# Kernel tuning notes

Hardware: AMD Instinct MI355X
Metric: run time of the kernel (lower is better)

The kernel has to match this reference:

```python
import jax, jax.numpy as jnp
import numpy as np

B, T, C = 2, 2048, 1024
H = 16
HS = C // H  # 64
LN_EPS = 1e-5

def setup_inputs() -> dict:
    key = jax.random.key(0)
    ks = jax.random.split(key, 12)
    s = lambda *sh: 0.02
    inp = {
        'x': jax.random.normal(ks[0], (B, T, C), jnp.float32),
        # per-head Q/K/V weights (bias=False), stacked over heads: [H, C, HS]
        'wq': jax.random.normal(ks[1], (H, C, HS), jnp.float32) * 0.02,
        'wk': jax.random.normal(ks[2], (H, C, HS), jnp.float32) * 0.02,
        'wv': jax.random.normal(ks[3], (H, C, HS), jnp.float32) * 0.02,
        'w_proj': jax.random.normal(ks[4], (C, C), jnp.float32) * 0.02,
        'b_proj': jnp.zeros((C,), jnp.float32),
        'w1': jax.random.normal(ks[5], (C, 4 * C), jnp.float32) * 0.02,
        'b1': jnp.zeros((4 * C,), jnp.float32),
        'w2': jax.random.normal(ks[6], (4 * C, C), jnp.float32) * 0.02,
        'b2': jnp.zeros((C,), jnp.float32),
        'ln1_g': jnp.ones((C,), jnp.float32),
        'ln1_b': jnp.zeros((C,), jnp.float32),
        'ln2_g': jnp.ones((C,), jnp.float32),
        'ln2_b': jnp.zeros((C,), jnp.float32),
    }
    return inp

def _layernorm(x, g, b):
    mu = jnp.mean(x, axis=-1, keepdims=True)
    var = jnp.mean(jnp.square(x - mu), axis=-1, keepdims=True)
    return (x - mu) * jax.lax.rsqrt(var + LN_EPS) * g + b

def reference(x, wq, wk, wv, w_proj, b_proj, w1, b1, w2, b2, ln1_g, ln1_b, ln2_g, ln2_b):
    Bx, Tx, Cx = x.shape
    h = _layernorm(x, ln1_g, ln1_b)
    q = jnp.einsum('btc,hcd->bhtd', h, wq)
    k = jnp.einsum('btc,hcd->bhtd', h, wk)
    v = jnp.einsum('btc,hcd->bhtd', h, wv)
    # NOTE: original scales by n_embedding**-0.5 (C), not head_size**-0.5
    scores = jnp.einsum('bhtd,bhsd->bhts', q, k) * (Cx ** -0.5)
    causal = jnp.tril(jnp.ones((Tx, Tx), bool))
    scores = jnp.where(causal, scores, -jnp.inf)
    att = jax.nn.softmax(scores, axis=-1)  # [B,H,T,T]
    out = jnp.einsum('bhts,bhsd->bhtd', att, v)
    out = out.transpose(0, 2, 1, 3).reshape(Bx, Tx, Cx)  # concat heads
    out = out @ w_proj + b_proj
    x = x + out
    h2 = _layernorm(x, ln2_g, ln2_b)
    ff = jax.nn.relu(h2 @ w1 + b1) @ w2 + b2
    return x + ff
```

## Files before the change

### kernel.cpp

```cpp
#include <hip/hip_runtime.h>
#include <hip/hip_bf16.h>
#include <stdint.h>

typedef __bf16 bf16_t;
typedef __bf16 bf16x8 __attribute__((ext_vector_type(8)));
typedef __bf16 bf16x4 __attribute__((ext_vector_type(4)));
typedef float f32x4 __attribute__((ext_vector_type(4)));

static constexpr int TT = 2048, CC = 1024;

__device__ __forceinline__ void gld_lds16(const void* g, void* l) {
  __builtin_amdgcn_global_load_lds((const __attribute__((address_space(1))) void*)g,
                                   (__attribute__((address_space(3))) void*)l, 16, 0, 0);
}

__global__ __launch_bounds__(256) void prep_all(const float* __restrict__ wq,
                                                const float* __restrict__ wk,
                                                const float* __restrict__ wv,
                                                const float* __restrict__ wproj,
                                                const float* __restrict__ w1,
                                                const float* __restrict__ w2,
                                                bf16_t* __restrict__ Bqkv,
                                                bf16_t* __restrict__ Bproj,
                                                bf16_t* __restrict__ B1w,
                                                bf16_t* __restrict__ B2w,
                                                const float* __restrict__ x,
                                                const float* __restrict__ g,
                                                const float* __restrict__ b,
                                                bf16_t* __restrict__ h1out) {
  const int id = blockIdx.x;
  const int tid = threadIdx.x;
  if (id >= 12288) {
    const int row = id - 12288;
    const float4 v = ((const float4*)(x + (size_t)row * CC))[tid];
    float s = v.x + v.y + v.z + v.w;
    float q = v.x * v.x + v.y * v.y + v.z * v.z + v.w * v.w;
#pragma unroll
    for (int off = 1; off < 64; off <<= 1) {
      s += __shfl_xor(s, off);
      q += __shfl_xor(q, off);
    }
    __shared__ float red[8];
    const int wave = tid >> 6, lane = tid & 63;
    if (lane == 0) { red[wave] = s; red[4 + wave] = q; }
    __syncthreads();
    s = red[0] + red[1] + red[2] + red[3];
    q = red[4] + red[5] + red[6] + red[7];
    const float mu = s * (1.0f / CC);
    float var = q * (1.0f / CC) - mu * mu;
    var = fmaxf(var, 0.f);
    const float rstd = rsqrtf(var + 1e-5f);
    const float4 gv = ((const float4*)g)[tid];
    const float4 bv = ((const float4*)b)[tid];
    bf16x4 o;
    o[0] = (bf16_t)((v.x - mu) * rstd * gv.x + bv.x);
    o[1] = (bf16_t)((v.y - mu) * rstd * gv.y + bv.y);
    o[2] = (bf16_t)((v.z - mu) * rstd * gv.z + bv.z);
    o[3] = (bf16_t)((v.w - mu) * rstd * gv.w + bv.w);
    *(bf16x4*)(h1out + (size_t)row * CC + tid * 4) = o;
    return;
  }
  const float* in;
  bf16_t* out;
  int K, N, kb, nb;
  if (id < 3072) {
    const int which = id >> 10;
    const int r = id & 1023;
    const int z = r >> 6;
    const int rr = r & 63;
    kb = rr >> 1;
    nb = rr & 1;
    K = 1024; N = 64;
    const float* srcs[3] = {wq, wk, wv};
    in = srcs[which] + (size_t)z * 1024 * 64;
    out = Bqkv + (size_t)which * 1024 * 1024 + (size_t)z * 1024 * 64;
  } else if (id < 4096) {
    const int r = id - 3072;
    kb = r >> 5; nb = r & 31;
    K = 1024; N = 1024;
    in = wproj; out = Bproj;
  } else if (id < 8192) {
    const int r = id - 4096;
    kb = r & 31; nb = r >> 5;
    K = 1024; N = 4096;
    in = w1; out = B1w;
  } else {
    const int r = id - 8192;
    kb = r >> 5; nb = r & 31;
    K = 4096; N = 1024;
    in = w2; out = B2w;
  }
  __shared__ float t[32][33];
  const int tx = tid & 31, ty = tid >> 5;
  const int k0 = kb * 32, n0 = nb * 32;
#pragma unroll
  for (int j = 0; j < 4; ++j)
    t[ty + j * 8][tx] = in[(size_t)(k0 + ty + j * 8) * N + n0 + tx];
  __syncthreads();
#pragma unroll
  for (int j = 0; j < 4; ++j)
    out[(size_t)(n0 + ty + j * 8) * K + k0 + tx] = (bf16_t)t[tx][ty + j * 8];
}

__global__ __launch_bounds__(256) void ln_f32_bf16(const float* __restrict__ x,
                                                   const float* __restrict__ g,
                                                   const float* __restrict__ b,
                                                   bf16_t* __restrict__ out) {
  const int row = blockIdx.x;
  const int tid = threadIdx.x;
  const float4 v = ((const float4*)(x + (size_t)row * CC))[tid];
  float s = v.x + v.y + v.z + v.w;
  float q = v.x * v.x + v.y * v.y + v.z * v.z + v.w * v.w;
#pragma unroll
  for (int off = 1; off < 64; off <<= 1) {
    s += __shfl_xor(s, off);
    q += __shfl_xor(q, off);
  }
  __shared__ float red[8];
  const int wave = tid >> 6, lane = tid & 63;
  if (lane == 0) { red[wave] = s; red[4 + wave] = q; }
  __syncthreads();
  s = red[0] + red[1] + red[2] + red[3];
  q = red[4] + red[5] + red[6] + red[7];
  const float mu = s * (1.0f / CC);
  float var = q * (1.0f / CC) - mu * mu;
  var = fmaxf(var, 0.f);
  const float rstd = rsqrtf(var + 1e-5f);
  const float4 gv = ((const float4*)g)[tid];
  const float4 bv = ((const float4*)b)[tid];
  bf16x4 o;
  o[0] = (bf16_t)((v.x - mu) * rstd * gv.x + bv.x);
  o[1] = (bf16_t)((v.y - mu) * rstd * gv.y + bv.y);
  o[2] = (bf16_t)((v.z - mu) * rstd * gv.z + bv.z);
  o[3] = (bf16_t)((v.w - mu) * rstd * gv.w + bv.w);
  *(bf16x4*)(out + (size_t)row * CC + tid * 4) = o;
}

template <int EPI, int BM, int BN, int DEPTH, int NW>
__global__ __launch_bounds__(NW * 64) void gemm_bt(const bf16_t* __restrict__ A,
                                                   const bf16_t* __restrict__ Bt,
                                                   void* __restrict__ Cout,
                                                   const float* __restrict__ bias,
                                                   const float* __restrict__ res,
                                                   bf16_t* __restrict__ vt,
                                                   int M, int N, int K) {
  constexpr int WSN = (NW == 8) ? 4 : 2;
  constexpr int WM = BM / 2, WN = BN / WSN;
  constexpr int MF = WM / 16, NF = WN / 16;
  constexpr int WROWS = NW * 8;
  constexpr int NA = BM / WROWS, NB = BN / WROWS;
  __shared__ alignas(16) bf16_t As[DEPTH][BM * 64];
  __shared__ alignas(16) bf16_t Bs[DEPTH][BN * 64];
  const int tid = threadIdx.x;
  const int wave = tid >> 6, lane = tid & 63;
  const int lr = lane & 15, lg = lane >> 4;
  const int wm = wave / WSN, wn = wave % WSN;

  const int gx = gridDim.x;
  const int nwg = gx * gridDim.y;
  const int orig = (int)blockIdx.y * gx + (int)blockIdx.x;
  const int wgid = (orig & 7) * (nwg >> 3) + (orig >> 3);
  const int tm0 = (wgid / gx) * BM, tn0 = (wgid % gx) * BN;

  const int sr = lane >> 3;
  const int scs = (lane & 7) ^ sr;
  const bf16_t* Ag[NA];
#pragma unroll
  for (int i = 0; i < NA; ++i)
    Ag[i] = A + (size_t)(tm0 + i * WROWS + wave * 8 + sr) * K + scs * 8;
  const bf16_t* Bg[NB];
#pragma unroll
  for (int i = 0; i < NB; ++i)
    Bg[i] = Bt + (size_t)(tn0 + i * WROWS + wave * 8 + sr) * K + scs * 8;

  auto STAGE = [&](int k0, int buf) {
#pragma unroll
    for (int i = 0; i < NA; ++i)
      gld_lds16(Ag[i] + k0, &As[buf][(i * WROWS + wave * 8) * 64]);
#pragma unroll
    for (int i = 0; i < NB; ++i)
      gld_lds16(Bg[i] + k0, &Bs[buf][(i * WROWS + wave * 8) * 64]);
  };

  f32x4 acc[MF][NF] = {};
  const int NT = K >> 6;

  STAGE(0, 0);
  asm volatile("s_waitcnt vmcnt(0)" ::: "memory");
  __builtin_amdgcn_s_barrier();

  for (int t = 0; t < NT; ++t) {
    const int cur = t % DEPTH;
    const bf16_t* Ac = As[cur];
    const bf16_t* Bc = Bs[cur];
    const bool more = (t + DEPTH - 1) < NT;
    if (more) STAGE((t + DEPTH - 1) << 6, (t + DEPTH - 1) % DEPTH);

    __builtin_amdgcn_s_setprio(1);
#pragma unroll
    for (int kk = 0; kk < 2; ++kk) {
      const int ch = ((kk * 4 + lg) ^ (lr & 7)) * 8;
      bf16x8 af[MF], bfr[NF];
#pragma unroll
      for (int n = 0; n < NF; ++n)
        bfr[n] = *(const bf16x8*)&Bc[(wn * WN + n * 16 + lr) * 64 + ch];
#pragma unroll
      for (int m = 0; m < MF; ++m)
        af[m] = *(const bf16x8*)&Ac[(wm * WM + m * 16 + lr) * 64 + ch];
#pragma unroll
      for (int m = 0; m < MF; ++m)
#pragma unroll
        for (int n = 0; n < NF; ++n)
          acc[m][n] =
              __builtin_amdgcn_mfma_f32_16x16x32_bf16(af[m], bfr[n], acc[m][n], 0, 0, 0);
    }
    __builtin_amdgcn_s_setprio(0);
    asm volatile("s_waitcnt vmcnt(0)" ::: "memory");
    __builtin_amdgcn_sched_barrier(0);
    __builtin_amdgcn_s_barrier();
  }

#pragma unroll
  for (int m = 0; m < MF; ++m) {
#pragma unroll
    for (int i = 0; i < 4; ++i) {
      const int row = tm0 + wm * WM + m * 16 + lg * 4 + i;
#pragma unroll
      for (int n = 0; n < NF; ++n) {
        const int col = tn0 + wn * WN + n * 16 + lr;
        float v = acc[m][n][i];
        if (EPI == 1) v = fmaxf(v + bias[col], 0.f);
        if (EPI == 2) v = v + bias[col] + res[(size_t)row * N + col];
        if (EPI == 2) {
          ((float*)Cout)[(size_t)row * N + col] = v;
        } else if (EPI == 3) {
          if (col >= 2048) {
            const int hd = col - 2048;
            const size_t vidx =
                ((size_t)((row >> 11) * 16 + (hd >> 6)) * 64 + (hd & 63)) * TT + (row & (TT - 1));
            vt[vidx] = (bf16_t)v;
          } else {
            ((bf16_t*)Cout)[(size_t)row * N + col] = (bf16_t)v;
          }
        } else {
          ((bf16_t*)Cout)[(size_t)row * N + col] = (bf16_t)v;
        }
      }
    }
  }
}

__global__ __launch_bounds__(256, 3) void attn_fwd(const bf16_t* __restrict__ qkv,
                                                   const bf16_t* __restrict__ Vt,
                                                   bf16_t* __restrict__ O) {
  const int bh = blockIdx.x;
  const int bb = bh >> 4, hh = bh & 15;
  const int qt = 31 - (int)blockIdx.y;
  const int qbase = qt * 64;
  const int tid = threadIdx.x;
  const int wave = tid >> 6, lane = tid & 63;
  const int lr = lane & 15, lg = lane >> 4;
  const bf16_t* Qp = qkv + (size_t)bb * TT * 3072 + hh * 64;
  const bf16_t* Kp = Qp + 1024;
  const bf16_t* Vh = Vt + (size_t)bh * 64 * TT;

  constexpr int KLP = 72;
  constexpr int VLP = 136;
  constexpr int PLP = 136;
  __shared__ alignas(16) bf16_t Klds[128 * KLP];
  __shared__ alignas(16) bf16_t Vlds[64 * VLP];
  __shared__ alignas(16) bf16_t PlS[4][16 * PLP];
  bf16_t* Pw = PlS[wave];

  const int ksr = wave * 32 + (lane >> 3);
  const int ksc = (lane & 7) * 8;
  const int vsr = wave * 16 + (lane >> 4);
  const int vsc = (lane & 15) * 8;

  const int qrow = qbase + wave * 16;
  bf16x8 qf0, qf1;
  {
    const bf16x8 a = *(const bf16x8*)(Qp + (size_t)(qrow + lr) * 3072 + lg * 8);
    const bf16x8 b = *(const bf16x8*)(Qp + (size_t)(qrow + lr) * 3072 + 32 + lg * 8);
#pragma unroll
    for (int j = 0; j < 8; ++j) {
      qf0[j] = (bf16_t)((float)a[j] * 0.03125f);
      qf1[j] = (bf16_t)((float)b[j] * 0.03125f);
    }
  }

  f32x4 oacc[4] = {};
  float m_r[4], l_r[4];
#pragma unroll
  for (int i = 0; i < 4; ++i) { m_r[i] = -1e38f; l_r[i] = 0.f; }

  bf16x8 kpre[4], vpre[4];
#pragma unroll
  for (int i = 0; i < 4; ++i) {
    kpre[i] = *(const bf16x8*)(Kp + (size_t)(ksr + i * 8) * 3072 + ksc);
    vpre[i] = *(const bf16x8*)(Vh + (size_t)(vsr + i * 4) * TT + vsc);
  }
#pragma unroll
  for (int i = 0; i < 4; ++i) {
    *(bf16x8*)&Klds[(ksr + i * 8) * KLP + ksc] = kpre[i];
    *(bf16x8*)&Vlds[(vsr + i * 4) * VLP + vsc] = vpre[i];
  }
  __syncthreads();

  const int nt = (qt >> 1) + 1;
  for (int t = 0; t < nt; ++t) {
    const int s0 = t * 128;
    const int sn = (t + 1 < nt) ? s0 + 128 : s0;
#pragma unroll
    for (int i = 0; i < 4; ++i) {
      kpre[i] = *(const bf16x8*)(Kp + (size_t)(sn + ksr + i * 8) * 3072 + ksc);
      vpre[i] = *(const bf16x8*)(Vh + (size_t)(vsr + i * 4) * TT + sn + vsc);
    }

    const int u = (qrow - s0) >> 4;
    const int cmc = min(u | 1, 7);

    float P[8][4];
    __builtin_amdgcn_s_setprio(1);
#pragma unroll
    for (int ct = 0; ct < 8; ++ct) {
      if (ct <= cmc) {
        const bf16x8 kf0 = *(const bf16x8*)&Klds[(ct * 16 + lr) * KLP + lg * 8];
        const bf16x8 kf1 = *(const bf16x8*)&Klds[(ct * 16 + lr) * KLP + 32 + lg * 8];
        f32x4 z = {};
        z = __builtin_amdgcn_mfma_f32_16x16x32_bf16(qf0, kf0, z, 0, 0, 0);
        z = __builtin_amdgcn_mfma_f32_16x16x32_bf16(qf1, kf1, z, 0, 0, 0);
        if (ct >= u) {
          const int sg = s0 + ct * 16 + lr;
#pragma unroll
          for (int i = 0; i < 4; ++i)
            P[ct][i] = (sg > qrow + lg * 4 + i) ? -1e30f : z[i];
        } else {
#pragma unroll
          for (int i = 0; i < 4; ++i) P[ct][i] = z[i];
        }
      } else {
#pragma unroll
        for (int i = 0; i < 4; ++i) P[ct][i] = -1e30f;
      }
    }
    __builtin_amdgcn_s_setprio(0);

    float lmax[4];
#pragma unroll
    for (int i = 0; i < 4; ++i) {
      float m0 = fmaxf(fmaxf(P[0][i], P[1][i]), fmaxf(P[2][i], P[3][i]));
      float m1 = fmaxf(fmaxf(P[4][i], P[5][i]), fmaxf(P[6][i], P[7][i]));
      lmax[i] = fmaxf(m0, m1);
    }
    const bool ok = (lmax[0] <= m_r[0] + 8.f) && (lmax[1] <= m_r[1] + 8.f) &&
                    (lmax[2] <= m_r[2] + 8.f) && (lmax[3] <= m_r[3] + 8.f);
    if (!__all(ok)) {
      float rm[4] = {lmax[0], lmax[1], lmax[2], lmax[3]};
#pragma unroll
      for (int off = 1; off < 16; off <<= 1)
#pragma unroll
        for (int i = 0; i < 4; ++i) rm[i] = fmaxf(rm[i], __shfl_xor(rm[i], off));
#pragma unroll
      for (int i = 0; i < 4; ++i) {
        const float mn = fmaxf(m_r[i], rm[i]);
        const float alpha = __expf(m_r[i] - mn);
        m_r[i] = mn;
        l_r[i] *= alpha;
#pragma unroll
        for (int db = 0; db < 4; ++db) oacc[db][i] *= alpha;
      }
    }

#pragma unroll
    for (int i = 0; i < 4; ++i) {
      float ls = 0.f;
#pragma unroll
      for (int ct = 0; ct < 8; ++ct) {
        const float p = __expf(P[ct][i] - m_r[i]);
        P[ct][i] = p;
        ls += p;
      }
      l_r[i] += ls;
    }

#pragma unroll
    for (int ct = 0; ct < 8; ++ct) {
      if (ct <= cmc) {
#pragma unroll
        for (int i = 0; i < 4; ++i) {
          const int q = lg * 4 + i;
          const int col = (ct * 16 + lr) ^ ((lg >> 1) << 4);
          Pw[q * PLP + col] = (bf16_t)P[ct][i];
        }
      }
    }
    asm volatile("s_waitcnt lgkmcnt(0)" ::: "memory");
    __builtin_amdgcn_sched_barrier(0);

    const int kcm = cmc >> 1;
    __builtin_amdgcn_s_setprio(1);
#pragma unroll
    for (int kc = 0; kc < 4; ++kc) {
      if (kc <= kcm) {
        const bf16x8 pf =
            *(const bf16x8*)&Pw[lr * PLP + ((kc * 32 + lg * 8) ^ ((lr >> 3) << 4))];
#pragma unroll
        for (int db = 0; db < 4; ++db) {
          const bf16x8 vf = *(const bf16x8*)&Vlds[(db * 16 + lr) * VLP + kc * 32 + lg * 8];
          oacc[db] = __builtin_amdgcn_mfma_f32_16x16x32_bf16(pf, vf, oacc[db], 0, 0, 0);
        }
      }
    }
    __builtin_amdgcn_s_setprio(0);

    if (t + 1 < nt) {
      __syncthreads();
#pragma unroll
      for (int i = 0; i < 4; ++i) {
        *(bf16x8*)&Klds[(ksr + i * 8) * KLP + ksc] = kpre[i];
        *(bf16x8*)&Vlds[(vsr + i * 4) * VLP + vsc] = vpre[i];
      }
      __syncthreads();
    }
  }

#pragma unroll
  for (int off = 1; off < 16; off <<= 1)
#pragma unroll
    for (int i = 0; i < 4; ++i) l_r[i] += __shfl_xor(l_r[i], off);

  bf16_t* Op = O + ((size_t)bb * TT + qrow) * CC + hh * 64;
#pragma unroll
  for (int i = 0; i < 4; ++i) {
    const float rl = 1.0f / l_r[i];
#pragma unroll
    for (int db = 0; db < 4; ++db)
      Op[(size_t)(lg * 4 + i) * CC + db * 16 + lr] = (bf16_t)(oacc[db][i] * rl);
  }
}

extern "C" void kernel_launch(void* const* d_in, const int* in_sizes, int n_in,
                              void* d_out, int out_size, void* d_ws, size_t ws_size,
                              hipStream_t stream) {
  const float* x      = (const float*)d_in[0];
  const float* wq     = (const float*)d_in[1];
  const float* wk     = (const float*)d_in[2];
  const float* wv     = (const float*)d_in[3];
  const float* w_proj = (const float*)d_in[4];
  const float* b_proj = (const float*)d_in[5];
  const float* w1     = (const float*)d_in[6];
  const float* b1     = (const float*)d_in[7];
  const float* w2     = (const float*)d_in[8];
  const float* b2     = (const float*)d_in[9];
  const float* ln1_g  = (const float*)d_in[10];
  const float* ln1_b  = (const float*)d_in[11];
  const float* ln2_g  = (const float*)d_in[12];
  const float* ln2_b  = (const float*)d_in[13];

  char* ws = (char*)d_ws;
  const size_t MB = 1024 * 1024;
  bf16_t* h1    = (bf16_t*)(ws + 0);
  bf16_t* Bqkv  = (bf16_t*)(ws + 8 * MB);
  bf16_t* Bproj = (bf16_t*)(ws + 14 * MB);
  bf16_t* B1w   = (bf16_t*)(ws + 16 * MB);
  bf16_t* B2w   = (bf16_t*)(ws + 24 * MB);
  bf16_t* qkv   = (bf16_t*)(ws + 32 * MB);
  bf16_t* Obuf  = (bf16_t*)(ws + 56 * MB);
  float*  res1  = (float*)(ws + 64 * MB);
  bf16_t* Vt    = (bf16_t*)(ws + 64 * MB);
  bf16_t* h2    = (bf16_t*)(ws + 80 * MB);
  bf16_t* a1    = (bf16_t*)(ws + 32 * MB);
  float*  outp  = (float*)d_out;

  dim3 blk(256), blk512(512);
  prep_all<<<dim3(16384), blk, 0, stream>>>(wq, wk, wv, w_proj, w1, w2,
                                            Bqkv, Bproj, B1w, B2w,
                                            x, ln1_g, ln1_b, h1);

  gemm_bt<3, 128, 128, 2, 8><<<dim3(24, 32), blk512, 0, stream>>>(h1, Bqkv, qkv, nullptr,
                                                                  nullptr, Vt, 4096, 3072, 1024);
  attn_fwd<<<dim3(32, 32), blk, 0, stream>>>(qkv, Vt, Obuf);
  gemm_bt<2, 64, 64, 2, 4><<<dim3(16, 64), blk, 0, stream>>>(Obuf, Bproj, res1, b_proj, x,
                                                             nullptr, 4096, 1024, 1024);
  ln_f32_bf16<<<dim3(4096), blk, 0, stream>>>(res1, ln2_g, ln2_b, h2);
  gemm_bt<1, 128, 128, 2, 8><<<dim3(32, 32), blk512, 0, stream>>>(h2, B1w, a1, b1, nullptr,
                                                                  nullptr, 4096, 4096, 1024);
  gemm_bt<2, 64, 64, 2, 4><<<dim3(16, 64), blk, 0, stream>>>(a1, B2w, outp, b2, res1,
                                                             nullptr, 4096, 1024, 4096);
}
```

Measured before the change: 237.6 us.

## Load V fragments directly from global into registers, drop V LDS staging

The attention kernel no longer stages V tiles through shared memory. Each wave now loads its 16 V fragments for the current key tile straight from global memory into registers at the start of the tile, and feeds them to the PV MFMAs. This removes the V LDS buffer and its stores, shrinking LDS use so the launch bound can target 4 blocks per SU instead of 3. In exchange, each of the four waves redundantly reads the full V tile from global/L2, and the loads are no longer prefetched a tile ahead. The 64 extra VGPRs per lane for V fragments may pressure registers under the tighter occupancy bound.

```diff
diff --git a/kernel.cpp b/kernel.cpp
--- a/kernel.cpp
+++ b/kernel.cpp
@@ -250,7 +250,7 @@
   }
 }
 
-__global__ __launch_bounds__(256, 3) void attn_fwd(const bf16_t* __restrict__ qkv,
+__global__ __launch_bounds__(256, 4) void attn_fwd(const bf16_t* __restrict__ qkv,
                                                    const bf16_t* __restrict__ Vt,
                                                    bf16_t* __restrict__ O) {
   const int bh = blockIdx.x;
@@ -265,17 +265,13 @@
   const bf16_t* Vh = Vt + (size_t)bh * 64 * TT;
 
   constexpr int KLP = 72;
-  constexpr int VLP = 136;
   constexpr int PLP = 136;
   __shared__ alignas(16) bf16_t Klds[128 * KLP];
-  __shared__ alignas(16) bf16_t Vlds[64 * VLP];
   __shared__ alignas(16) bf16_t PlS[4][16 * PLP];
   bf16_t* Pw = PlS[wave];
 
   const int ksr = wave * 32 + (lane >> 3);
   const int ksc = (lane & 7) * 8;
-  const int vsr = wave * 16 + (lane >> 4);
-  const int vsc = (lane & 15) * 8;
 
   const int qrow = qbase + wave * 16;
   bf16x8 qf0, qf1;
@@ -294,17 +290,13 @@
 #pragma unroll
   for (int i = 0; i < 4; ++i) { m_r[i] = -1e38f; l_r[i] = 0.f; }
 
-  bf16x8 kpre[4], vpre[4];
-#pragma unroll
-  for (int i = 0; i < 4; ++i) {
+  bf16x8 kpre[4];
+#pragma unroll
+  for (int i = 0; i < 4; ++i)
     kpre[i] = *(const bf16x8*)(Kp + (size_t)(ksr + i * 8) * 3072 + ksc);
-    vpre[i] = *(const bf16x8*)(Vh + (size_t)(vsr + i * 4) * TT + vsc);
-  }
-#pragma unroll
-  for (int i = 0; i < 4; ++i) {
+#pragma unroll
+  for (int i = 0; i < 4; ++i)
     *(bf16x8*)&Klds[(ksr + i * 8) * KLP + ksc] = kpre[i];
-    *(bf16x8*)&Vlds[(vsr + i * 4) * VLP + vsc] = vpre[i];
-  }
   __syncthreads();
 
   const int nt = (qt >> 1) + 1;
@@ -312,10 +304,16 @@
     const int s0 = t * 128;
     const int sn = (t + 1 < nt) ? s0 + 128 : s0;
 #pragma unroll
-    for (int i = 0; i < 4; ++i) {
+    for (int i = 0; i < 4; ++i)
       kpre[i] = *(const bf16x8*)(Kp + (size_t)(sn + ksr + i * 8) * 3072 + ksc);
-      vpre[i] = *(const bf16x8*)(Vh + (size_t)(vsr + i * 4) * TT + sn + vsc);
-    }
+
+    bf16x8 vf[4][4];
+#pragma unroll
+    for (int kc = 0; kc < 4; ++kc)
+#pragma unroll
+      for (int db = 0; db < 4; ++db)
+        vf[kc][db] =
+            *(const bf16x8*)(Vh + (size_t)(db * 16 + lr) * TT + s0 + kc * 32 + lg * 8);
 
     const int u = (qrow - s0) >> 4;
     const int cmc = min(u | 1, 7);
@@ -406,10 +404,8 @@
         const bf16x8 pf =
             *(const bf16x8*)&Pw[lr * PLP + ((kc * 32 + lg * 8) ^ ((lr >> 3) << 4))];
 #pragma unroll
-        for (int db = 0; db < 4; ++db) {
-          const bf16x8 vf = *(const bf16x8*)&Vlds[(db * 16 + lr) * VLP + kc * 32 + lg * 8];
-          oacc[db] = __builtin_amdgcn_mfma_f32_16x16x32_bf16(pf, vf, oacc[db], 0, 0, 0);
-        }
+        for (int db = 0; db < 4; ++db)
+          oacc[db] = __builtin_amdgcn_mfma_f32_16x16x32_bf16(pf, vf[kc][db], oacc[db], 0, 0, 0);
       }
     }
     __builtin_amdgcn_s_setprio(0);
@@ -417,10 +413,8 @@
     if (t + 1 < nt) {
       __syncthreads();
 #pragma unroll
-      for (int i = 0; i < 4; ++i) {
+      for (int i = 0; i < 4; ++i)
         *(bf16x8*)&Klds[(ksr + i * 8) * KLP + ksc] = kpre[i];
-        *(bf16x8*)&Vlds[(vsr + i * 4) * VLP + vsc] = vpre[i];
-      }
       __syncthreads();
     }
   }
```

Result: slower. 381.9 us (+60.8%).
